# Kernel tuning notes

Measured on AMD Instinct MI355X. Metric: run time of the kernel, lower is better.

## Reference

```python
import jax, jax.numpy as jnp
import numpy as np

N_NODES = 20000
N_EDGES = 400000
IN_DIM = 512
OUT_DIM = 1
HIDDEN = [512, 512, 512, 256, OUT_DIM]


def _glorot(key, fan_in, fan_out):
    lim = np.sqrt(6.0 / (fan_in + fan_out)).astype(np.float32)
    return jax.random.uniform(key, (fan_in, fan_out), jnp.float32, -lim, lim)


def setup_inputs() -> dict:
    key = jax.random.key(0)
    ks = jax.random.split(key, 16)
    x = jax.random.normal(ks[0], (N_NODES, IN_DIM), jnp.float32)
    edge_index = jax.random.randint(ks[1], (2, N_EDGES), 0, N_NODES, jnp.int64)
    edge_attr = jax.random.uniform(ks[2], (N_EDGES,), jnp.float32)
    inp = {"x": x, "edge_index": edge_index, "edge_attr": edge_attr}
    dims = [IN_DIM] + HIDDEN
    for i in range(5):
        inp[f"W{i+1}"] = _glorot(ks[3 + i], dims[i], dims[i + 1])
        inp[f"b{i+1}"] = jnp.zeros((dims[i + 1],), jnp.float32)
    return inp


def gcn_layer(x, W, b, src, dst, ew, n):
    # x: [N, Fin] -> [N, Fout]; GCNConv: D^{-1/2}(A+I)D^{-1/2} X W + b
    h = x @ W
    loop = jnp.arange(n)
    src_f = jnp.concatenate([src, loop])
    dst_f = jnp.concatenate([dst, loop])
    ew_f = jnp.concatenate([ew, jnp.ones((n,), x.dtype)])  # self-loop weight 1
    deg = jax.ops.segment_sum(ew_f, dst_f, num_segments=n)
    dinv = jnp.where(deg > 0, jax.lax.rsqrt(deg), 0.0)
    norm = dinv[src_f] * ew_f * dinv[dst_f]  # [E+N]
    out = jax.ops.segment_sum(norm[:, None] * h[src_f], dst_f, num_segments=n)
    return out + b


def reference(x, edge_index, edge_attr, W1, b1, W2, b2, W3, b3, W4, b4, W5, b5):
    src, dst = edge_index[0], edge_index[1]
    n = x.shape[0]
    h = jax.nn.relu(gcn_layer(x, W1, b1, src, dst, edge_attr, n))
    h = jax.nn.relu(gcn_layer(h, W2, b2, src, dst, edge_attr, n))
    h = jax.nn.relu(gcn_layer(h, W3, b3, src, dst, edge_attr, n))
    h = jax.nn.relu(gcn_layer(h, W4, b4, src, dst, edge_attr, n))
    h = gcn_layer(h, W5, b5, src, dst, edge_attr, n)
    return h
```

## Files before the change

kernel.cpp:

```cpp
#include <hip/hip_runtime.h>
#include <cstdint>
#include <cstddef>

#define N_NODES 20000
#define N_EDGES 400000
#define NBLK 79
#define MPAD 20128

typedef __attribute__((ext_vector_type(8))) short bf16x8;
typedef __attribute__((ext_vector_type(4))) float f32x4;

__device__ __forceinline__ float bf2f(unsigned short u) {
    return __uint_as_float(((unsigned int)u) << 16);
}
__device__ __forceinline__ unsigned short f2bf(float f) {
    unsigned int x = __float_as_uint(f);
    unsigned int lsb = (x >> 16) & 1u;
    x += 0x7fffu + lsb;
    return (unsigned short)(x >> 16);
}

__device__ __forceinline__ float ldF(const void* p, size_t i, bool bf) {
    return bf ? bf2f(((const unsigned short*)p)[i]) : ((const float*)p)[i];
}

__device__ __forceinline__ void gl2lds16(const unsigned short* g, unsigned short* l) {
    __builtin_amdgcn_global_load_lds(
        (const __attribute__((address_space(1))) void*)g,
        (__attribute__((address_space(3))) void*)l, 16, 0, 0);
}

__global__ void k_detect(const unsigned int* __restrict__ xw, const int* __restrict__ raw,
                         int* __restrict__ flag) {
    int lane = threadIdx.x;
    int cnt = 0, nz = 0;
    for (int i = lane; i < 256; i += 64) {
        unsigned short lo = (unsigned short)(xw[i] & 0xffffu);
        int e = (lo >> 7) & 0xff;
        if (e >= 110 && e <= 135) cnt++;
    }
    for (int i = 2 * lane + 1; i < 512; i += 128)
        if (raw[i] != 0) nz++;
#pragma unroll
    for (int off = 32; off > 0; off >>= 1) {
        cnt += __shfl_down(cnt, off);
        nz  += __shfl_down(nz, off);
    }
    if (lane == 0) {
        flag[0] = (cnt >= 128) ? 1 : 0;
        flag[1] = (nz == 0) ? 1 : 0;
    }
}

__global__ void k_canon_deg(const int* __restrict__ raw, const void* __restrict__ ew,
                            const int* __restrict__ flagp,
                            int* __restrict__ src32, int* __restrict__ dst32,
                            float* __restrict__ deg, int* __restrict__ counts) {
    bool bf = (flagp[0] != 0);
    int is64 = flagp[1];
    int e = blockIdx.x * blockDim.x + threadIdx.x;
    if (e >= N_EDGES) return;
    int s, d;
    if (is64) { s = raw[2 * e]; d = raw[2 * (N_EDGES + e)]; }
    else      { s = raw[e];     d = raw[N_EDGES + e]; }
    src32[e] = s;
    dst32[e] = d;
    atomicAdd(&deg[d], ldF(ew, e, bf));
    atomicAdd(&counts[d], 1);
}

__global__ __launch_bounds__(256) void k_part(const int* __restrict__ counts,
                                              const float* __restrict__ deg,
                                              float* __restrict__ dinv,
                                              float* __restrict__ selfnorm,
                                              int* __restrict__ bsum) {
    __shared__ int s[256];
    int t = threadIdx.x;
    int i = blockIdx.x * 256 + t;
    int c = (i < N_NODES) ? counts[i] : 0;
    if (i < N_NODES) {
        float d = deg[i] + 1.0f;
        float r = rsqrtf(d);
        dinv[i] = r;
        selfnorm[i] = r * r;
    }
    s[t] = c;
    __syncthreads();
    for (int off = 128; off > 0; off >>= 1) {
        if (t < off) s[t] += s[t + off];
        __syncthreads();
    }
    if (t == 0) bsum[blockIdx.x] = s[0];
}

__global__ void k_scanb(const int* __restrict__ bsum, int* __restrict__ bofs,
                        int* __restrict__ rowptr) {
    __shared__ int s[128];
    int t = threadIdx.x;
    int v = (t < NBLK) ? bsum[t] : 0;
    s[t] = v;
    __syncthreads();
    for (int off = 1; off < 128; off <<= 1) {
        int u = (t >= off) ? s[t - off] : 0;
        __syncthreads();
        s[t] += u;
        __syncthreads();
    }
    if (t < NBLK) bofs[t] = s[t] - v;
    if (t == NBLK - 1) rowptr[N_NODES] = s[t];
}

__global__ __launch_bounds__(256) void k_row(const int* __restrict__ counts,
                                             const int* __restrict__ bofs,
                                             int* __restrict__ rowptr) {
    __shared__ int s[256];
    int t = threadIdx.x;
    int b = blockIdx.x;
    int i = b * 256 + t;
    int c = (i < N_NODES) ? counts[i] : 0;
    s[t] = c;
    __syncthreads();
    for (int off = 1; off < 256; off <<= 1) {
        int u = (t >= off) ? s[t - off] : 0;
        __syncthreads();
        s[t] += u;
        __syncthreads();
    }
    if (i < N_NODES) rowptr[i] = bofs[b] + s[t] - c;
}

__global__ void k_csr(const int* __restrict__ src, const int* __restrict__ dst,
                      const void* __restrict__ ew, const int* __restrict__ flagp,
                      const float* __restrict__ dinv, const int* __restrict__ rowptr,
                      int* __restrict__ fill, int* __restrict__ csr_src,
                      float* __restrict__ csr_norm) {
    bool bf = (*flagp != 0);
    int e = blockIdx.x * blockDim.x + threadIdx.x;
    if (e >= N_EDGES) return;
    int s = src[e], d = dst[e];
    int p = rowptr[d] + atomicAdd(&fill[d], 1);
    csr_src[p] = s;
    csr_norm[p] = dinv[s] * ldF(ew, e, bf) * dinv[d];
}

__global__ __launch_bounds__(256) void k_prep(const void* __restrict__ x,
                                              const void* __restrict__ W1,
                                              const void* __restrict__ W2,
                                              const void* __restrict__ W3,
                                              const void* __restrict__ W4,
                                              const void* __restrict__ b1,
                                              const void* __restrict__ b2,
                                              const void* __restrict__ b3,
                                              const void* __restrict__ b4,
                                              const void* __restrict__ W5,
                                              const int* __restrict__ flagp,
                                              unsigned short* __restrict__ P,
                                              unsigned short* __restrict__ Wp,
                                              float* __restrict__ biasf) {
    bool bf = (*flagp != 0);
    int b = blockIdx.x;
    int t = threadIdx.x;
    if (b < 10000) {
        int i = b * 256 + t;
        if (bf) {
            ((uint2*)P)[i] = ((const uint2*)x)[i];
        } else {
            float4 v = ((const float4*)x)[i];
            unsigned int lo = (unsigned int)f2bf(v.x) | ((unsigned int)f2bf(v.y) << 16);
            unsigned int hi = (unsigned int)f2bf(v.z) | ((unsigned int)f2bf(v.w) << 16);
            ((uint2*)P)[i] = make_uint2(lo, hi);
        }
    } else if (b < 10448) {
        int gidx = (b - 10000) * 256 + t;
        if (gidx >= 114688) return;
        const void* W;
        int idx = gidx, N, nbl;
        if (gidx < 32768)      { W = W1; N = 512; nbl = 5; }
        else if (gidx < 65536) { W = W2; N = 512; nbl = 5; idx -= 32768; }
        else if (gidx < 98304) { W = W3; N = 512; nbl = 5; idx -= 65536; }
        else                   { W = W4; N = 256; nbl = 4; idx -= 98304; }
        int lane = idx & 63;
        int blk = idx >> 6;
        int nb = blk & ((1 << nbl) - 1);
        int kb = blk >> nbl;
        int n = (nb << 4) + (lane & 15);
        int kbase = (kb << 5) + ((lane >> 4) << 3);
        unsigned short o[8];
#pragma unroll
        for (int j = 0; j < 8; ++j)
            o[j] = f2bf(ldF(W, (size_t)(kbase + j) * N + n, bf));
        *(uint4*)(&Wp[(size_t)gidx * 8]) = *(const uint4*)o;
    } else {
        int i = (b - 10448) * 256 + t;
        if (i >= 2304) return;
        if (i < 2048) {
            int L = i >> 9, r = i & 511;
            if (L == 3 && r >= 256) return;
            const void* bb = (L == 0) ? b1 : (L == 1) ? b2 : (L == 2) ? b3 : b4;
            biasf[i] = ldF(bb, r, bf);
        } else {
            biasf[i] = ldF(W5, i - 2048, bf);
        }
    }
}

__global__ __launch_bounds__(256) void k_gemm_mfma(const unsigned short* __restrict__ A,
                                                   const unsigned short* __restrict__ Bp,
                                                   unsigned short* __restrict__ C,
                                                   int M, int K, int N) {
    const int AP = 72;
    __shared__ __align__(16) unsigned short As[128 * AP];
    __shared__ __align__(16) unsigned short Bs[2 * 8 * 512];
    int tid = threadIdx.x;
    int lane = tid & 63;
    int wave = tid >> 6;
    int wr = wave >> 1, wc = wave & 1;
    int row0 = blockIdx.x * 128;
    int col0 = blockIdx.y * 128;
    int nbt = N >> 4;
    int q = lane >> 4;
    int mm = lane & 15;

    f32x4 acc[4][4] = {};

    for (int kb2 = 0; kb2 < (K >> 6); ++kb2) {
        const unsigned short* breg0 = Bp + (((size_t)(2 * kb2) * nbt + (col0 >> 4)) << 9);
        const unsigned short* breg1 = Bp + (((size_t)(2 * kb2 + 1) * nbt + (col0 >> 4)) << 9);
        gl2lds16(breg0 + (size_t)tid * 8, &Bs[(size_t)tid * 8]);
        gl2lds16(breg0 + (size_t)(tid + 256) * 8, &Bs[(size_t)(tid + 256) * 8]);
        gl2lds16(breg1 + (size_t)tid * 8, &Bs[4096 + (size_t)tid * 8]);
        gl2lds16(breg1 + (size_t)(tid + 256) * 8, &Bs[4096 + (size_t)(tid + 256) * 8]);
#pragma unroll
        for (int i = 0; i < 4; ++i) {
            int c = tid + i * 256;
            int row = c >> 3, kq = c & 7;
            uint4 v = *(const uint4*)(&A[(size_t)(row0 + row) * K + (kb2 << 6) + (kq << 3)]);
            *(uint4*)(&As[row * AP + (kq << 3)]) = v;
        }
        __syncthreads();
#pragma unroll
        for (int kk = 0; kk < 2; ++kk) {
            bf16x8 af[4], bfr[4];
#pragma unroll
            for (int mb = 0; mb < 4; ++mb)
                af[mb] = *(const bf16x8*)(&As[(wr * 64 + mb * 16 + mm) * AP + kk * 32 + q * 8]);
#pragma unroll
            for (int nb = 0; nb < 4; ++nb)
                bfr[nb] = *(const bf16x8*)(&Bs[kk * 4096 + ((wc * 4 + nb) * 64 + lane) * 8]);
#pragma unroll
            for (int mb = 0; mb < 4; ++mb)
#pragma unroll
                for (int nb = 0; nb < 4; ++nb)
                    acc[mb][nb] = __builtin_amdgcn_mfma_f32_16x16x32_bf16(
                        af[mb], bfr[nb], acc[mb][nb], 0, 0, 0);
        }
        __syncthreads();
    }
#pragma unroll
    for (int mb = 0; mb < 4; ++mb) {
#pragma unroll
        for (int r = 0; r < 4; ++r) {
            int grow = row0 + wr * 64 + mb * 16 + q * 4 + r;
            if (grow < M) {
#pragma unroll
                for (int nb = 0; nb < 4; ++nb) {
                    int gcol = col0 + wc * 64 + nb * 16 + mm;
                    C[(size_t)grow * N + gcol] = f2bf(acc[mb][nb][r]);
                }
            }
        }
    }
}

template <int W>
__device__ __forceinline__ void ldrow(const unsigned short* h, size_t row, int F, int lane,
                                      unsigned int* u) {
    const unsigned int* p = (const unsigned int*)(h + row * F) + lane * W;
    if constexpr (W == 4) {
        uint4 v = *(const uint4*)p; u[0] = v.x; u[1] = v.y; u[2] = v.z; u[3] = v.w;
    } else {
        uint2 v = *(const uint2*)p; u[0] = v.x; u[1] = v.y;
    }
}
template <int W>
__device__ __forceinline__ void fmarow(const unsigned int* u, float w, float* acc) {
#pragma unroll
    for (int k = 0; k < W; ++k) {
        acc[2 * k]     = fmaf(bf2f((unsigned short)(u[k] & 0xffffu)), w, acc[2 * k]);
        acc[2 * k + 1] = fmaf(bf2f((unsigned short)(u[k] >> 16)),     w, acc[2 * k + 1]);
    }
}

__global__ __launch_bounds__(256) void k_agg_w(const unsigned short* __restrict__ h,
                                               const int* __restrict__ rowptr,
                                               const int* __restrict__ csr_src,
                                               const float* __restrict__ csr_norm,
                                               const float* __restrict__ selfnorm,
                                               const float* __restrict__ biasf,
                                               unsigned short* __restrict__ out) {
    constexpr int F = 512, FPL = 8, W = 4;
    int lane = threadIdx.x & 63;
    int wave = threadIdx.x >> 6;
    int node = blockIdx.x * 4 + wave;
    if (node >= N_NODES) return;
    int e0 = rowptr[node], e1 = rowptr[node + 1];
    float sn = selfnorm[node];

    float acc[FPL];
    {
        unsigned int u[W];
        ldrow<W>(h, (size_t)node, F, lane, u);
#pragma unroll
        for (int k = 0; k < W; ++k) {
            acc[2 * k]     = sn * bf2f((unsigned short)(u[k] & 0xffffu));
            acc[2 * k + 1] = sn * bf2f((unsigned short)(u[k] >> 16));
        }
    }
    int j = e0;
    for (; j + 3 < e1; j += 4) {
        int s0 = csr_src[j], s1 = csr_src[j + 1], s2 = csr_src[j + 2], s3 = csr_src[j + 3];
        float w0 = csr_norm[j], w1 = csr_norm[j + 1], w2 = csr_norm[j + 2], w3 = csr_norm[j + 3];
        unsigned int u0[W], u1[W], u2[W], u3[W];
        ldrow<W>(h, (size_t)s0, F, lane, u0);
        ldrow<W>(h, (size_t)s1, F, lane, u1);
        ldrow<W>(h, (size_t)s2, F, lane, u2);
        ldrow<W>(h, (size_t)s3, F, lane, u3);
        fmarow<W>(u0, w0, acc);
        fmarow<W>(u1, w1, acc);
        fmarow<W>(u2, w2, acc);
        fmarow<W>(u3, w3, acc);
    }
    for (; j < e1; ++j) {
        int s0 = csr_src[j];
        float w0 = csr_norm[j];
        unsigned int u0[W];
        ldrow<W>(h, (size_t)s0, F, lane, u0);
        fmarow<W>(u0, w0, acc);
    }
    {
        const float* bp = biasf + lane * FPL;
#pragma unroll
        for (int k = 0; k < FPL; ++k) acc[k] = fmaxf(acc[k] + bp[k], 0.f);
        unsigned int o[W];
#pragma unroll
        for (int k = 0; k < W; ++k)
            o[k] = (unsigned int)f2bf(acc[2 * k]) | ((unsigned int)f2bf(acc[2 * k + 1]) << 16);
        *(uint4*)((unsigned int*)(out + (size_t)node * F) + lane * W) =
            make_uint4(o[0], o[1], o[2], o[3]);
    }
}

__global__ __launch_bounds__(256) void k_agg_fuse(const unsigned short* __restrict__ h,
                                                  const int* __restrict__ rowptr,
                                                  const int* __restrict__ csr_src,
                                                  const float* __restrict__ csr_norm,
                                                  const float* __restrict__ selfnorm,
                                                  const float* __restrict__ biasf,
                                                  const float* __restrict__ w5f,
                                                  float* __restrict__ h5) {
    constexpr int F = 256, FPL = 4, W = 2;
    int lane = threadIdx.x & 63;
    int wave = threadIdx.x >> 6;
    int node = blockIdx.x * 4 + wave;
    if (node >= N_NODES) return;
    int e0 = rowptr[node], e1 = rowptr[node + 1];
    float sn = selfnorm[node];

    float acc[FPL];
    {
        unsigned int u[W];
        ldrow<W>(h, (size_t)node, F, lane, u);
#pragma unroll
        for (int k = 0; k < W; ++k) {
            acc[2 * k]     = sn * bf2f((unsigned short)(u[k] & 0xffffu));
            acc[2 * k + 1] = sn * bf2f((unsigned short)(u[k] >> 16));
        }
    }
    int j = e0;
    for (; j + 3 < e1; j += 4) {
        int s0 = csr_src[j], s1 = csr_src[j + 1], s2 = csr_src[j + 2], s3 = csr_src[j + 3];
        float w0 = csr_norm[j], w1 = csr_norm[j + 1], w2 = csr_norm[j + 2], w3 = csr_norm[j + 3];
        unsigned int u0[W], u1[W], u2[W], u3[W];
        ldrow<W>(h, (size_t)s0, F, lane, u0);
        ldrow<W>(h, (size_t)s1, F, lane, u1);
        ldrow<W>(h, (size_t)s2, F, lane, u2);
        ldrow<W>(h, (size_t)s3, F, lane, u3);
        fmarow<W>(u0, w0, acc);
        fmarow<W>(u1, w1, acc);
        fmarow<W>(u2, w2, acc);
        fmarow<W>(u3, w3, acc);
    }
    for (; j < e1; ++j) {
        int s0 = csr_src[j];
        float w0 = csr_norm[j];
        unsigned int u0[W];
        ldrow<W>(h, (size_t)s0, F, lane, u0);
        fmarow<W>(u0, w0, acc);
    }
    const float* bp = biasf + lane * FPL;
    const float* wp = w5f + lane * FPL;
    float partial = 0.f;
#pragma unroll
    for (int k = 0; k < FPL; ++k)
        partial += fmaxf(acc[k] + bp[k], 0.f) * wp[k];
#pragma unroll
    for (int off = 32; off > 0; off >>= 1)
        partial += __shfl_xor(partial, off);
    if (lane == 0) h5[node] = partial;
}

__global__ void k_final(const float* __restrict__ h5, const int* __restrict__ rowptr,
                        const int* __restrict__ csr_src, const float* __restrict__ csr_norm,
                        const float* __restrict__ selfnorm,
                        const void* __restrict__ b5, const int* __restrict__ flagp,
                        void* __restrict__ out) {
    bool bf = (*flagp != 0);
    int i = blockIdx.x * blockDim.x + threadIdx.x;
    if (i >= N_NODES) return;
    float acc = selfnorm[i] * h5[i];
    int e0 = rowptr[i], e1 = rowptr[i + 1];
    for (int j = e0; j < e1; ++j) acc += csr_norm[j] * h5[csr_src[j]];
    acc += ldF(b5, 0, bf);
    if (bf) ((unsigned short*)out)[i] = f2bf(acc);
    else    ((float*)out)[i] = acc;
}

extern "C" void kernel_launch(void* const* d_in, const int* in_sizes, int n_in,
                              void* d_out, int out_size, void* d_ws, size_t ws_size,
                              hipStream_t stream) {
    const void* x  = d_in[0];
    const int*  ei = (const int*)d_in[1];
    const void* ea = d_in[2];
    const void* W1 = d_in[3];
    const void* b1 = d_in[4];
    const void* W2 = d_in[5];
    const void* b2 = d_in[6];
    const void* W3 = d_in[7];
    const void* b3 = d_in[8];
    const void* W4 = d_in[9];
    const void* b4 = d_in[10];
    const void* W5 = d_in[11];
    const void* b5 = d_in[12];

    char* ws = (char*)d_ws;
    size_t off = 0;
    auto take = [&](size_t bytes) -> void* {
        off = (off + 255) & ~(size_t)255;
        void* p = ws + off;
        off += bytes;
        return p;
    };
    int*   flagp    = (int*)take(2 * sizeof(int));
    float* deg      = (float*)take(N_NODES * sizeof(float));
    int*   counts   = (int*)take(N_NODES * sizeof(int));
    int*   fill     = (int*)take(N_NODES * sizeof(int));
    size_t zspan    = (size_t)((char*)(fill + N_NODES) - (char*)deg);
    float* dinv     = (float*)take(N_NODES * sizeof(float));
    float* selfnorm = (float*)take(N_NODES * sizeof(float));
    float* h5       = (float*)take(N_NODES * sizeof(float));
    float* biasf    = (float*)take(2304 * sizeof(float));
    int*   bsum     = (int*)take(128 * sizeof(int));
    int*   bofs     = (int*)take(128 * sizeof(int));
    int*   rowptr   = (int*)take((N_NODES + 1) * sizeof(int));
    int*   src32    = (int*)take(N_EDGES * sizeof(int));
    int*   dst32    = (int*)take(N_EDGES * sizeof(int));
    int*   csr_src  = (int*)take(N_EDGES * sizeof(int));
    float* csr_norm = (float*)take(N_EDGES * sizeof(float));
    unsigned short* Wp = (unsigned short*)take((size_t)114688 * 8 * sizeof(unsigned short));
    unsigned short* P  = (unsigned short*)take((size_t)MPAD * 512 * sizeof(unsigned short));
    unsigned short* H  = (unsigned short*)take((size_t)MPAD * 512 * sizeof(unsigned short));

    hipMemsetAsync(deg, 0, zspan, stream);

    const int EB = (N_EDGES + 255) / 256;
    const int NB = (N_NODES + 255) / 256;
    const int AGB = (N_NODES + 3) / 4;

    k_detect<<<1, 64, 0, stream>>>((const unsigned int*)x, ei, flagp);
    k_canon_deg<<<EB, 256, 0, stream>>>(ei, ea, flagp, src32, dst32, deg, counts);
    k_part<<<NB, 256, 0, stream>>>(counts, deg, dinv, selfnorm, bsum);
    k_scanb<<<1, 128, 0, stream>>>(bsum, bofs, rowptr);
    k_row<<<NB, 256, 0, stream>>>(counts, bofs, rowptr);
    k_csr<<<EB, 256, 0, stream>>>(src32, dst32, ea, flagp, dinv, rowptr, fill, csr_src, csr_norm);

    k_prep<<<10457, 256, 0, stream>>>(x, W1, W2, W3, W4, b1, b2, b3, b4, W5, flagp,
                                      P, Wp, biasf);

    const int MB128 = (N_NODES + 127) / 128;

    k_gemm_mfma<<<dim3(MB128, 4), 256, 0, stream>>>(P, Wp, H, N_NODES, 512, 512);
    k_agg_w<<<AGB, 256, 0, stream>>>(H, rowptr, csr_src, csr_norm, selfnorm, biasf, P);
    k_gemm_mfma<<<dim3(MB128, 4), 256, 0, stream>>>(P, Wp + (size_t)32768 * 8, H,
                                                    N_NODES, 512, 512);
    k_agg_w<<<AGB, 256, 0, stream>>>(H, rowptr, csr_src, csr_norm, selfnorm, biasf + 512, P);
    k_gemm_mfma<<<dim3(MB128, 4), 256, 0, stream>>>(P, Wp + (size_t)65536 * 8, H,
                                                    N_NODES, 512, 512);
    k_agg_w<<<AGB, 256, 0, stream>>>(H, rowptr, csr_src, csr_norm, selfnorm, biasf + 1024, P);
    k_gemm_mfma<<<dim3(MB128, 2), 256, 0, stream>>>(P, Wp + (size_t)98304 * 8, H,
                                                    N_NODES, 512, 256);
    k_agg_fuse<<<AGB, 256, 0, stream>>>(H, rowptr, csr_src, csr_norm, selfnorm,
                                        biasf + 1536, biasf + 2048, h5);

    k_final<<<NB, 256, 0, stream>>>(h5, rowptr, csr_src, csr_norm, selfnorm, b5, flagp,
                                    d_out);
}
```

Baseline: 458.5 us.

## Interleave CSR src/norm pairs, drop edge staging arrays, skip bf16 input copy

Packs each CSR entry's source index and normalized weight into one 8-byte pair, so the aggregation kernels issue one nontemporal vector load per edge instead of two scalar loads from separate arrays. The canonicalisation kernel no longer writes src32/dst32; k_csr reads the raw edge index directly. When the input is already bf16, the first GEMM reads x in place and the copy into P is skipped. To support that, GEMM row loads are clamped to M-1. The data path for the default fp32 input barely changes, so most of the benefit comes from the paired loads and less preprocessing traffic.

```diff
diff --git a/kernel.cpp b/kernel.cpp
--- a/kernel.cpp
+++ b/kernel.cpp
@@ -9,6 +9,7 @@
 
 typedef __attribute__((ext_vector_type(8))) short bf16x8;
 typedef __attribute__((ext_vector_type(4))) float f32x4;
+typedef __attribute__((ext_vector_type(2))) int i32x2;
 
 __device__ __forceinline__ float bf2f(unsigned short u) {
     return __uint_as_float(((unsigned int)u) << 16);
@@ -54,17 +55,14 @@
 
 __global__ void k_canon_deg(const int* __restrict__ raw, const void* __restrict__ ew,
                             const int* __restrict__ flagp,
-                            int* __restrict__ src32, int* __restrict__ dst32,
                             float* __restrict__ deg, int* __restrict__ counts) {
     bool bf = (flagp[0] != 0);
     int is64 = flagp[1];
     int e = blockIdx.x * blockDim.x + threadIdx.x;
     if (e >= N_EDGES) return;
-    int s, d;
-    if (is64) { s = raw[2 * e]; d = raw[2 * (N_EDGES + e)]; }
-    else      { s = raw[e];     d = raw[N_EDGES + e]; }
-    src32[e] = s;
-    dst32[e] = d;
+    int d;
+    if (is64) d = raw[2 * (N_EDGES + e)];
+    else      d = raw[N_EDGES + e];
     atomicAdd(&deg[d], ldF(ew, e, bf));
     atomicAdd(&counts[d], 1);
 }
@@ -129,18 +127,23 @@
     if (i < N_NODES) rowptr[i] = bofs[b] + s[t] - c;
 }
 
-__global__ void k_csr(const int* __restrict__ src, const int* __restrict__ dst,
-                      const void* __restrict__ ew, const int* __restrict__ flagp,
+__global__ void k_csr(const int* __restrict__ raw, const void* __restrict__ ew,
+                      const int* __restrict__ flagp,
                       const float* __restrict__ dinv, const int* __restrict__ rowptr,
-                      int* __restrict__ fill, int* __restrict__ csr_src,
-                      float* __restrict__ csr_norm) {
-    bool bf = (*flagp != 0);
+                      int* __restrict__ fill, int* __restrict__ csr_pair) {
+    bool bf = (flagp[0] != 0);
+    int is64 = flagp[1];
     int e = blockIdx.x * blockDim.x + threadIdx.x;
     if (e >= N_EDGES) return;
-    int s = src[e], d = dst[e];
+    int s, d;
+    if (is64) { s = raw[2 * e]; d = raw[2 * (N_EDGES + e)]; }
+    else      { s = raw[e];     d = raw[N_EDGES + e]; }
     int p = rowptr[d] + atomicAdd(&fill[d], 1);
-    csr_src[p] = s;
-    csr_norm[p] = dinv[s] * ldF(ew, e, bf) * dinv[d];
+    float nrm = dinv[s] * ldF(ew, e, bf) * dinv[d];
+    i32x2 pv;
+    pv.x = s;
+    pv.y = __float_as_int(nrm);
+    *(i32x2*)(csr_pair + 2 * (size_t)p) = pv;
 }
 
 __global__ __launch_bounds__(256) void k_prep(const void* __restrict__ x,
@@ -161,15 +164,12 @@
     int b = blockIdx.x;
     int t = threadIdx.x;
     if (b < 10000) {
+        if (bf) return;
         int i = b * 256 + t;
-        if (bf) {
-            ((uint2*)P)[i] = ((const uint2*)x)[i];
-        } else {
-            float4 v = ((const float4*)x)[i];
-            unsigned int lo = (unsigned int)f2bf(v.x) | ((unsigned int)f2bf(v.y) << 16);
-            unsigned int hi = (unsigned int)f2bf(v.z) | ((unsigned int)f2bf(v.w) << 16);
-            ((uint2*)P)[i] = make_uint2(lo, hi);
-        }
+        float4 v = ((const float4*)x)[i];
+        unsigned int lo = (unsigned int)f2bf(v.x) | ((unsigned int)f2bf(v.y) << 16);
+        unsigned int hi = (unsigned int)f2bf(v.z) | ((unsigned int)f2bf(v.w) << 16);
+        ((uint2*)P)[i] = make_uint2(lo, hi);
     } else if (b < 10448) {
         int gidx = (b - 10000) * 256 + t;
         if (gidx >= 114688) return;
@@ -204,13 +204,16 @@
     }
 }
 
-__global__ __launch_bounds__(256) void k_gemm_mfma(const unsigned short* __restrict__ A,
+__global__ __launch_bounds__(256) void k_gemm_mfma(const unsigned short* __restrict__ Abase,
+                                                   const unsigned short* __restrict__ Aalt,
+                                                   const int* __restrict__ flagp,
                                                    const unsigned short* __restrict__ Bp,
                                                    unsigned short* __restrict__ C,
                                                    int M, int K, int N) {
     const int AP = 72;
     __shared__ __align__(16) unsigned short As[128 * AP];
     __shared__ __align__(16) unsigned short Bs[2 * 8 * 512];
+    const unsigned short* A = (*flagp != 0) ? Aalt : Abase;
     int tid = threadIdx.x;
     int lane = tid & 63;
     int wave = tid >> 6;
@@ -234,7 +237,8 @@
         for (int i = 0; i < 4; ++i) {
             int c = tid + i * 256;
             int row = c >> 3, kq = c & 7;
-            uint4 v = *(const uint4*)(&A[(size_t)(row0 + row) * K + (kb2 << 6) + (kq << 3)]);
+            int grow = min(row0 + row, M - 1);
+            uint4 v = *(const uint4*)(&A[(size_t)grow * K + (kb2 << 6) + (kq << 3)]);
             *(uint4*)(&As[row * AP + (kq << 3)]) = v;
         }
         __syncthreads();
@@ -293,8 +297,7 @@
 
 __global__ __launch_bounds__(256) void k_agg_w(const unsigned short* __restrict__ h,
                                                const int* __restrict__ rowptr,
-                                               const int* __restrict__ csr_src,
-                                               const float* __restrict__ csr_norm,
+                                               const int* __restrict__ csr_pair,
                                                const float* __restrict__ selfnorm,
                                                const float* __restrict__ biasf,
                                                unsigned short* __restrict__ out) {
@@ -316,26 +319,28 @@
             acc[2 * k + 1] = sn * bf2f((unsigned short)(u[k] >> 16));
         }
     }
+    const i32x2* pairs = (const i32x2*)csr_pair;
     int j = e0;
     for (; j + 3 < e1; j += 4) {
-        int s0 = csr_src[j], s1 = csr_src[j + 1], s2 = csr_src[j + 2], s3 = csr_src[j + 3];
-        float w0 = csr_norm[j], w1 = csr_norm[j + 1], w2 = csr_norm[j + 2], w3 = csr_norm[j + 3];
+        i32x2 p0 = __builtin_nontemporal_load(pairs + j);
+        i32x2 p1 = __builtin_nontemporal_load(pairs + j + 1);
+        i32x2 p2 = __builtin_nontemporal_load(pairs + j + 2);
+        i32x2 p3 = __builtin_nontemporal_load(pairs + j + 3);
         unsigned int u0[W], u1[W], u2[W], u3[W];
-        ldrow<W>(h, (size_t)s0, F, lane, u0);
-        ldrow<W>(h, (size_t)s1, F, lane, u1);
-        ldrow<W>(h, (size_t)s2, F, lane, u2);
-        ldrow<W>(h, (size_t)s3, F, lane, u3);
-        fmarow<W>(u0, w0, acc);
-        fmarow<W>(u1, w1, acc);
-        fmarow<W>(u2, w2, acc);
-        fmarow<W>(u3, w3, acc);
+        ldrow<W>(h, (size_t)p0.x, F, lane, u0);
+        ldrow<W>(h, (size_t)p1.x, F, lane, u1);
+        ldrow<W>(h, (size_t)p2.x, F, lane, u2);
+        ldrow<W>(h, (size_t)p3.x, F, lane, u3);
+        fmarow<W>(u0, __int_as_float(p0.y), acc);
+        fmarow<W>(u1, __int_as_float(p1.y), acc);
+        fmarow<W>(u2, __int_as_float(p2.y), acc);
+        fmarow<W>(u3, __int_as_float(p3.y), acc);
     }
     for (; j < e1; ++j) {
-        int s0 = csr_src[j];
-        float w0 = csr_norm[j];
+        i32x2 p0 = __builtin_nontemporal_load(pairs + j);
         unsigned int u0[W];
-        ldrow<W>(h, (size_t)s0, F, lane, u0);
-        fmarow<W>(u0, w0, acc);
+        ldrow<W>(h, (size_t)p0.x, F, lane, u0);
+        fmarow<W>(u0, __int_as_float(p0.y), acc);
     }
     {
         const float* bp = biasf + lane * FPL;
@@ -352,8 +357,7 @@
 
 __global__ __launch_bounds__(256) void k_agg_fuse(const unsigned short* __restrict__ h,
                                                   const int* __restrict__ rowptr,
-                                                  const int* __restrict__ csr_src,
-                                                  const float* __restrict__ csr_norm,
+                                                  const int* __restrict__ csr_pair,
                                                   const float* __restrict__ selfnorm,
                                                   const float* __restrict__ biasf,
                                                   const float* __restrict__ w5f,
@@ -376,26 +380,28 @@
             acc[2 * k + 1] = sn * bf2f((unsigned short)(u[k] >> 16));
         }
     }
+    const i32x2* pairs = (const i32x2*)csr_pair;
     int j = e0;
     for (; j + 3 < e1; j += 4) {
-        int s0 = csr_src[j], s1 = csr_src[j + 1], s2 = csr_src[j + 2], s3 = csr_src[j + 3];
-        float w0 = csr_norm[j], w1 = csr_norm[j + 1], w2 = csr_norm[j + 2], w3 = csr_norm[j + 3];
+        i32x2 p0 = __builtin_nontemporal_load(pairs + j);
+        i32x2 p1 = __builtin_nontemporal_load(pairs + j + 1);
+        i32x2 p2 = __builtin_nontemporal_load(pairs + j + 2);
+        i32x2 p3 = __builtin_nontemporal_load(pairs + j + 3);
         unsigned int u0[W], u1[W], u2[W], u3[W];
-        ldrow<W>(h, (size_t)s0, F, lane, u0);
-        ldrow<W>(h, (size_t)s1, F, lane, u1);
-        ldrow<W>(h, (size_t)s2, F, lane, u2);
-        ldrow<W>(h, (size_t)s3, F, lane, u3);
-        fmarow<W>(u0, w0, acc);
-        fmarow<W>(u1, w1, acc);
-        fmarow<W>(u2, w2, acc);
-        fmarow<W>(u3, w3, acc);
+        ldrow<W>(h, (size_t)p0.x, F, lane, u0);
+        ldrow<W>(h, (size_t)p1.x, F, lane, u1);
+        ldrow<W>(h, (size_t)p2.x, F, lane, u2);
+        ldrow<W>(h, (size_t)p3.x, F, lane, u3);
+        fmarow<W>(u0, __int_as_float(p0.y), acc);
+        fmarow<W>(u1, __int_as_float(p1.y), acc);
+        fmarow<W>(u2, __int_as_float(p2.y), acc);
+        fmarow<W>(u3, __int_as_float(p3.y), acc);
     }
     for (; j < e1; ++j) {
-        int s0 = csr_src[j];
-        float w0 = csr_norm[j];
+        i32x2 p0 = __builtin_nontemporal_load(pairs + j);
         unsigned int u0[W];
-        ldrow<W>(h, (size_t)s0, F, lane, u0);
-        fmarow<W>(u0, w0, acc);
+        ldrow<W>(h, (size_t)p0.x, F, lane, u0);
+        fmarow<W>(u0, __int_as_float(p0.y), acc);
     }
     const float* bp = biasf + lane * FPL;
     const float* wp = w5f + lane * FPL;
@@ -410,7 +416,7 @@
 }
 
 __global__ void k_final(const float* __restrict__ h5, const int* __restrict__ rowptr,
-                        const int* __restrict__ csr_src, const float* __restrict__ csr_norm,
+                        const int* __restrict__ csr_pair,
                         const float* __restrict__ selfnorm,
                         const void* __restrict__ b5, const int* __restrict__ flagp,
                         void* __restrict__ out) {
@@ -419,7 +425,11 @@
     if (i >= N_NODES) return;
     float acc = selfnorm[i] * h5[i];
     int e0 = rowptr[i], e1 = rowptr[i + 1];
-    for (int j = e0; j < e1; ++j) acc += csr_norm[j] * h5[csr_src[j]];
+    for (int j = e0; j < e1; ++j) {
+        int s = csr_pair[2 * (size_t)j];
+        float w = __int_as_float(csr_pair[2 * (size_t)j + 1]);
+        acc += w * h5[s];
+    }
     acc += ldF(b5, 0, bf);
     if (bf) ((unsigned short*)out)[i] = f2bf(acc);
     else    ((float*)out)[i] = acc;
@@ -462,45 +472,46 @@
     int*   bsum     = (int*)take(128 * sizeof(int));
     int*   bofs     = (int*)take(128 * sizeof(int));
     int*   rowptr   = (int*)take((N_NODES + 1) * sizeof(int));
-    int*   src32    = (int*)take(N_EDGES * sizeof(int));
-    int*   dst32    = (int*)take(N_EDGES * sizeof(int));
-    int*   csr_src  = (int*)take(N_EDGES * sizeof(int));
-    float* csr_norm = (float*)take(N_EDGES * sizeof(float));
+    int*   csr_pair = (int*)take((size_t)N_EDGES * 2 * sizeof(int));
     unsigned short* Wp = (unsigned short*)take((size_t)114688 * 8 * sizeof(unsigned short));
     unsigned short* P  = (unsigned short*)take((size_t)MPAD * 512 * sizeof(unsigned short));
     unsigned short* H  = (unsigned short*)take((size_t)MPAD * 512 * sizeof(unsigned short));
 
-    hipMemsetAsync(deg, 0, zspan, stream);
+    (void)hipMemsetAsync(deg, 0, zspan, stream);
 
     const int EB = (N_EDGES + 255) / 256;
     const int NB = (N_NODES + 255) / 256;
     const int AGB = (N_NODES + 3) / 4;
 
     k_detect<<<1, 64, 0, stream>>>((const unsigned int*)x, ei, flagp);
-    k_canon_deg<<<EB, 256, 0, stream>>>(ei, ea, flagp, src32, dst32, deg, counts);
+    k_canon_deg<<<EB, 256, 0, stream>>>(ei, ea, flagp, deg, counts);
     k_part<<<NB, 256, 0, stream>>>(counts, deg, dinv, selfnorm, bsum);
     k_scanb<<<1, 128, 0, stream>>>(bsum, bofs, rowptr);
     k_row<<<NB, 256, 0, stream>>>(counts, bofs, rowptr);
-    k_csr<<<EB, 256, 0, stream>>>(src32, dst32, ea, flagp, dinv, rowptr, fill, csr_src, csr_norm);
+    k_csr<<<EB, 256, 0, stream>>>(ei, ea, flagp, dinv, rowptr, fill, csr_pair);
 
     k_prep<<<10457, 256, 0, stream>>>(x, W1, W2, W3, W4, b1, b2, b3, b4, W5, flagp,
                                       P, Wp, biasf);
 
     const int MB128 = (N_NODES + 127) / 128;
 
-    k_gemm_mfma<<<dim3(MB128, 4), 256, 0, stream>>>(P, Wp, H, N_NODES, 512, 512);
-    k_agg_w<<<AGB, 256, 0, stream>>>(H, rowptr, csr_src, csr_norm, selfnorm, biasf, P);
-    k_gemm_mfma<<<dim3(MB128, 4), 256, 0, stream>>>(P, Wp + (size_t)32768 * 8, H,
+    k_gemm_mfma<<<dim3(MB128, 4), 256, 0, stream>>>(P, (const unsigned short*)x, flagp,
+                                                    Wp, H, N_NODES, 512, 512);
+    k_agg_w<<<AGB, 256, 0, stream>>>(H, rowptr, csr_pair, selfnorm, biasf, P);
+    k_gemm_mfma<<<dim3(MB128, 4), 256, 0, stream>>>(P, P, flagp,
+                                                    Wp + (size_t)32768 * 8, H,
                                                     N_NODES, 512, 512);
-    k_agg_w<<<AGB, 256, 0, stream>>>(H, rowptr, csr_src, csr_norm, selfnorm, biasf + 512, P);
-    k_gemm_mfma<<<dim3(MB128, 4), 256, 0, stream>>>(P, Wp + (size_t)65536 * 8, H,
+    k_agg_w<<<AGB, 256, 0, stream>>>(H, rowptr, csr_pair, selfnorm, biasf + 512, P);
+    k_gemm_mfma<<<dim3(MB128, 4), 256, 0, stream>>>(P, P, flagp,
+                                                    Wp + (size_t)65536 * 8, H,
                                                     N_NODES, 512, 512);
-    k_agg_w<<<AGB, 256, 0, stream>>>(H, rowptr, csr_src, csr_norm, selfnorm, biasf + 1024, P);
-    k_gemm_mfma<<<dim3(MB128, 2), 256, 0, stream>>>(P, Wp + (size_t)98304 * 8, H,
+    k_agg_w<<<AGB, 256, 0, stream>>>(H, rowptr, csr_pair, selfnorm, biasf + 1024, P);
+    k_gemm_mfma<<<dim3(MB128, 2), 256, 0, stream>>>(P, P, flagp,
+                                                    Wp + (size_t)98304 * 8, H,
                                                     N_NODES, 512, 256);
-    k_agg_fuse<<<AGB, 256, 0, stream>>>(H, rowptr, csr_src, csr_norm, selfnorm,
+    k_agg_fuse<<<AGB, 256, 0, stream>>>(H, rowptr, csr_pair, selfnorm,
                                         biasf + 1536, biasf + 2048, h5);
 
-    k_final<<<NB, 256, 0, stream>>>(h5, rowptr, csr_src, csr_norm, selfnorm, b5, flagp,
+    k_final<<<NB, 256, 0, stream>>>(h5, rowptr, csr_pair, selfnorm, b5, flagp,
                                     d_out);
 }
```

After: 474.2 us. 3.4% more time.
